# Performance work log

Measured on AMD Instinct MI355X. Metric: run time of the kernel, lower is better.

Reference implementation:

```python
import math
import jax, jax.numpy as jnp
import numpy as np

BATCH = 16384
N = 2048            # in_size = out_size, power of 2
LOG_N = 11          # log2(N)
NSTACKS = 1
NBLOCKS = 1


def setup_inputs() -> dict:
    key = jax.random.key(0)
    k1, k2, k3 = jax.random.split(key, 3)
    x = jax.random.normal(k1, (BATCH, N), jnp.float32)
    # init='randn': twiddle ~ N(0,1) / sqrt(2)
    twiddle = jax.random.normal(
        k2, (NSTACKS, NBLOCKS, LOG_N, N // 2, 2, 2), jnp.float32) / jnp.sqrt(jnp.float32(2.0))
    bound = 1.0 / math.sqrt(N)  # nn.Linear-style bias init, in_size = N
    bias = jax.random.uniform(k3, (N,), jnp.float32, -bound, bound)
    return {"x": x, "twiddle": twiddle, "bias": bias}


def butterfly_multiply(twiddle, x, increasing_stride=True):
    # twiddle: (S, n_blocks, log_n, n//2, 2, 2);  x: (B, S, n)
    B, S, n = x.shape
    n_blocks, log_n = twiddle.shape[1], twiddle.shape[2]
    out = x
    cur = increasing_stride
    for block in range(n_blocks):
        for idx in range(log_n):
            log_stride = idx if cur else log_n - 1 - idx
            s = 1 << log_stride
            g = n // (2 * s)  # number of butterfly groups at this stride
            # t: (S, g, s, 2, 2); pair axis j contracts against input halves
            t = twiddle[:, block, idx].reshape(S, g, s, 2, 2)
            xr = out.reshape(B, S, g, 2, s)
            out = jnp.einsum('kgsij,bkgjs->bkgis', t, xr).reshape(B, S, n)
        cur = not cur
    return out


def reference(x, twiddle, bias):
    B = x.shape[0]
    # pre_process: flatten batch dims, expand over nstacks
    out = jnp.broadcast_to(x[:, None, :], (B, NSTACKS, N))
    out = butterfly_multiply(twiddle, out, increasing_stride=True)
    # post_process: flatten stacks, truncate to out_size, add bias
    out = out.reshape(B, NSTACKS * N)[:, :N] + bias
    return out
```

## Files before the change

### kernel.cpp

```cpp
#include <hip/hip_runtime.h>


constexpr int BATCH = 16384;
constexpr int N = 2048;
constexpr int ROWS = 2;
constexpr int WPB = 4;
constexpr int BLOCK = 64 * WPB;
constexpr int GRID = BATCH / (ROWS * WPB);

#define SCHED_FENCE() asm volatile("" ::: "memory")

__device__ __forceinline__ int swz(int a) {
    return a ^ (((a >> 5) & 1) << 2) ^ (((a >> 6) & 1) << 3);
}

template <int M>
__device__ __forceinline__ float part_xor(float x) {
    if constexpr (M == 1)
        return __int_as_float(__builtin_amdgcn_mov_dpp(__float_as_int(x), 0xB1, 0xF, 0xF, true));
    else if constexpr (M == 2)
        return __int_as_float(__builtin_amdgcn_mov_dpp(__float_as_int(x), 0x4E, 0xF, 0xF, true));
    else if constexpr (M == 4)
        return __int_as_float(__builtin_amdgcn_ds_swizzle(__float_as_int(x), 0x101F));
    else if constexpr (M == 8)
        return __int_as_float(__builtin_amdgcn_ds_swizzle(__float_as_int(x), 0x201F));
    else if constexpr (M == 16)
        return __int_as_float(__builtin_amdgcn_ds_swizzle(__float_as_int(x), 0x401F));
    else
        return __shfl_xor(x, 32, 64);
}

template <int ST>
__device__ __forceinline__ void mid_stage(float (&v)[ROWS][32], const float* twb, int lane) {
    constexpr int s = 1 << ST;
    constexpr int m = 1 << (ST - 1);
    const int hiHalf = (lane >> (ST - 1)) & 1;
    const int l2 = lane * 2;
    #pragma unroll
    for (int k = 0; k < 32; ++k) {
        const int e = (k >> 1) * 128 + l2 + (k & 1);
        const int p = ((e >> (ST + 1)) << ST) | (e & (s - 1));
        const int a = swz(4 * p + 2 * hiHalf);
        const float2 t2 = *(const float2*)(twb + a);
        #pragma unroll
        for (int rr = 0; rr < ROWS; ++rr) {
            const float mine = v[rr][k];
            const float part = part_xor<m>(mine);
            const float lo = hiHalf ? part : mine;
            const float hi = hiHalf ? mine : part;
            v[rr][k] = fmaf(t2.x, lo, t2.y * hi);
        }
        if ((k & 3) == 3) SCHED_FENCE();
    }
}

template <int ST>
__device__ __forceinline__ void hi_stage(float (&v)[ROWS][32], const float* twb, int lane) {
    constexpr int s = 1 << ST;
    constexpr int rm = 1 << (ST - 7);
    const int l2 = lane * 2;
    #pragma unroll
    for (int r = 0; r < 16; ++r) {
        if (r & rm) continue;
        #pragma unroll
        for (int j = 0; j < 2; ++j) {
            const int e = r * 128 + l2 + j;
            const int p = ((e >> (ST + 1)) << ST) | (e & (s - 1));
            const int a = swz(4 * p);
            const float4 t4 = *(const float4*)(twb + a);
            const int klo = 2 * r + j;
            const int khi = 2 * (r + rm) + j;
            #pragma unroll
            for (int rr = 0; rr < ROWS; ++rr) {
                const float lo = v[rr][klo];
                const float hi = v[rr][khi];
                v[rr][klo] = fmaf(t4.x, lo, t4.y * hi);
                v[rr][khi] = fmaf(t4.z, lo, t4.w * hi);
            }
        }
        if ((r & 1) == 1) SCHED_FENCE();
    }
}

__global__ __launch_bounds__(BLOCK, 1)
void butterfly_kernel(const float* __restrict__ x,
                      const float* __restrict__ tw,
                      const float* __restrict__ bias,
                      float* __restrict__ out)
{
    __shared__ __align__(16) float lds[2][4096];
    const int tid = threadIdx.x;
    const int lane = tid & 63;
    const int w = tid >> 6;
    const int wid = blockIdx.x * WPB + w;
    const size_t row0 = (size_t)wid * ROWS;
    const int l2 = lane * 2;

    auto stage_tw = [&](int st, int buf) {
        const float* base = tw + (st << 12);
        #pragma unroll
        for (int i = 0; i < 4; ++i) {
            const int s = i * 256 + (w << 6) + lane;
            const int g = s ^ ((s >> 3) & 1) ^ (((s >> 4) & 1) << 1);
            __builtin_amdgcn_global_load_lds(
                (const __attribute__((address_space(1))) void*)(base + 4 * g),
                (__attribute__((address_space(3))) void*)(&lds[buf][(i * 256 + (w << 6)) * 4]),
                16, 0, 0);
        }
    };

    stage_tw(1, 1);

    float v[ROWS][32];

    #pragma unroll
    for (int rr = 0; rr < ROWS; ++rr) {
        const float* src = x + (row0 + rr) * N + l2;
        #pragma unroll
        for (int r = 0; r < 16; ++r) {
            const float2 f = *(const float2*)(src + r * 128);
            v[rr][2*r]   = f.x;
            v[rr][2*r+1] = f.y;
        }
    }

    #pragma unroll
    for (int r = 0; r < 16; ++r) {
        const float4 t4 = *(const float4*)(tw + 4 * (r * 64 + lane));
        #pragma unroll
        for (int rr = 0; rr < ROWS; ++rr) {
            const float lo = v[rr][2*r];
            const float hi = v[rr][2*r+1];
            v[rr][2*r]   = fmaf(t4.x, lo, t4.y * hi);
            v[rr][2*r+1] = fmaf(t4.z, lo, t4.w * hi);
        }
        if ((r & 3) == 3) SCHED_FENCE();
    }
    __syncthreads();

    stage_tw(2, 0);  mid_stage<1>(v, &lds[1][0], lane); __syncthreads();
    stage_tw(3, 1);  mid_stage<2>(v, &lds[0][0], lane); __syncthreads();
    stage_tw(4, 0);  mid_stage<3>(v, &lds[1][0], lane); __syncthreads();
    stage_tw(5, 1);  mid_stage<4>(v, &lds[0][0], lane); __syncthreads();
    stage_tw(6, 0);  mid_stage<5>(v, &lds[1][0], lane); __syncthreads();
    stage_tw(7, 1);  mid_stage<6>(v, &lds[0][0], lane); __syncthreads();
    stage_tw(8, 0);  hi_stage<7>(v, &lds[1][0], lane);  __syncthreads();
    stage_tw(9, 1);  hi_stage<8>(v, &lds[0][0], lane);  __syncthreads();
    stage_tw(10, 0); hi_stage<9>(v, &lds[1][0], lane);  __syncthreads();
    hi_stage<10>(v, &lds[0][0], lane);

    #pragma unroll
    for (int r = 0; r < 16; ++r) {
        const float2 b = *(const float2*)(bias + r * 128 + l2);
        #pragma unroll
        for (int rr = 0; rr < ROWS; ++rr) {
            float2 o;
            o.x = v[rr][2*r]   + b.x;
            o.y = v[rr][2*r+1] + b.y;
            *(float2*)(out + (row0 + rr) * N + r * 128 + l2) = o;
        }
    }
}

extern "C" void kernel_launch(void* const* d_in, const int* in_sizes, int n_in,
                              void* d_out, int out_size, void* d_ws, size_t ws_size,
                              hipStream_t stream) {
    const float* x    = (const float*)d_in[0];
    const float* tw   = (const float*)d_in[1];
    const float* bias = (const float*)d_in[2];
    float* out = (float*)d_out;

    butterfly_kernel<<<GRID, BLOCK, 0, stream>>>(x, tw, bias, out);
}
```

Baseline: 336.8 us.

## Read twiddles directly from global memory, drop LDS staging, process four rows per wave

Removes the double-buffered LDS staging of twiddle factors and the per-stage block barriers, so each wave loads twiddles directly from global memory (through cache). Rows per wave double to amortize each twiddle load over more batch rows, and the mid-stage butterfly precomputes per-lane coefficients to avoid selects. The trade-off is higher register pressure, fewer blocks, and exposing global/L2 latency on twiddle loads instead of LDS reads.

```diff
diff --git a/kernel.cpp b/kernel.cpp
--- a/kernel.cpp
+++ b/kernel.cpp
@@ -3,16 +3,12 @@
 
 constexpr int BATCH = 16384;
 constexpr int N = 2048;
-constexpr int ROWS = 2;
+constexpr int ROWS = 4;
 constexpr int WPB = 4;
 constexpr int BLOCK = 64 * WPB;
 constexpr int GRID = BATCH / (ROWS * WPB);
 
 #define SCHED_FENCE() asm volatile("" ::: "memory")
-
-__device__ __forceinline__ int swz(int a) {
-    return a ^ (((a >> 5) & 1) << 2) ^ (((a >> 6) & 1) << 3);
-}
 
 template <int M>
 __device__ __forceinline__ float part_xor(float x) {
@@ -31,7 +27,7 @@
 }
 
 template <int ST>
-__device__ __forceinline__ void mid_stage(float (&v)[ROWS][32], const float* twb, int lane) {
+__device__ __forceinline__ void mid_stage(float (&v)[ROWS][32], const float* twst, int lane) {
     constexpr int s = 1 << ST;
     constexpr int m = 1 << (ST - 1);
     const int hiHalf = (lane >> (ST - 1)) & 1;
@@ -40,22 +36,21 @@
     for (int k = 0; k < 32; ++k) {
         const int e = (k >> 1) * 128 + l2 + (k & 1);
         const int p = ((e >> (ST + 1)) << ST) | (e & (s - 1));
-        const int a = swz(4 * p + 2 * hiHalf);
-        const float2 t2 = *(const float2*)(twb + a);
+        const float2 t2 = *(const float2*)(twst + 4 * p + 2 * hiHalf);
+        const float cm = hiHalf ? t2.y : t2.x;
+        const float cp = hiHalf ? t2.x : t2.y;
         #pragma unroll
         for (int rr = 0; rr < ROWS; ++rr) {
             const float mine = v[rr][k];
             const float part = part_xor<m>(mine);
-            const float lo = hiHalf ? part : mine;
-            const float hi = hiHalf ? mine : part;
-            v[rr][k] = fmaf(t2.x, lo, t2.y * hi);
+            v[rr][k] = fmaf(cm, mine, cp * part);
         }
-        if ((k & 3) == 3) SCHED_FENCE();
+        if ((k & 7) == 7) SCHED_FENCE();
     }
 }
 
 template <int ST>
-__device__ __forceinline__ void hi_stage(float (&v)[ROWS][32], const float* twb, int lane) {
+__device__ __forceinline__ void hi_stage(float (&v)[ROWS][32], const float* twst, int lane) {
     constexpr int s = 1 << ST;
     constexpr int rm = 1 << (ST - 7);
     const int l2 = lane * 2;
@@ -66,8 +61,7 @@
         for (int j = 0; j < 2; ++j) {
             const int e = r * 128 + l2 + j;
             const int p = ((e >> (ST + 1)) << ST) | (e & (s - 1));
-            const int a = swz(4 * p);
-            const float4 t4 = *(const float4*)(twb + a);
+            const float4 t4 = *(const float4*)(twst + 4 * p);
             const int klo = 2 * r + j;
             const int khi = 2 * (r + rm) + j;
             #pragma unroll
@@ -88,28 +82,12 @@
                       const float* __restrict__ bias,
                       float* __restrict__ out)
 {
-    __shared__ __align__(16) float lds[2][4096];
     const int tid = threadIdx.x;
     const int lane = tid & 63;
     const int w = tid >> 6;
     const int wid = blockIdx.x * WPB + w;
     const size_t row0 = (size_t)wid * ROWS;
     const int l2 = lane * 2;
-
-    auto stage_tw = [&](int st, int buf) {
-        const float* base = tw + (st << 12);
-        #pragma unroll
-        for (int i = 0; i < 4; ++i) {
-            const int s = i * 256 + (w << 6) + lane;
-            const int g = s ^ ((s >> 3) & 1) ^ (((s >> 4) & 1) << 1);
-            __builtin_amdgcn_global_load_lds(
-                (const __attribute__((address_space(1))) void*)(base + 4 * g),
-                (__attribute__((address_space(3))) void*)(&lds[buf][(i * 256 + (w << 6)) * 4]),
-                16, 0, 0);
-        }
-    };
-
-    stage_tw(1, 1);
 
     float v[ROWS][32];
 
@@ -136,18 +114,18 @@
         }
         if ((r & 3) == 3) SCHED_FENCE();
     }
-    __syncthreads();
 
-    stage_tw(2, 0);  mid_stage<1>(v, &lds[1][0], lane); __syncthreads();
-    stage_tw(3, 1);  mid_stage<2>(v, &lds[0][0], lane); __syncthreads();
-    stage_tw(4, 0);  mid_stage<3>(v, &lds[1][0], lane); __syncthreads();
-    stage_tw(5, 1);  mid_stage<4>(v, &lds[0][0], lane); __syncthreads();
-    stage_tw(6, 0);  mid_stage<5>(v, &lds[1][0], lane); __syncthreads();
-    stage_tw(7, 1);  mid_stage<6>(v, &lds[0][0], lane); __syncthreads();
-    stage_tw(8, 0);  hi_stage<7>(v, &lds[1][0], lane);  __syncthreads();
-    stage_tw(9, 1);  hi_stage<8>(v, &lds[0][0], lane);  __syncthreads();
-    stage_tw(10, 0); hi_stage<9>(v, &lds[1][0], lane);  __syncthreads();
-    hi_stage<10>(v, &lds[0][0], lane);
+    mid_stage<1>(v, tw + (1 << 12), lane);
+    mid_stage<2>(v, tw + (2 << 12), lane);
+    mid_stage<3>(v, tw + (3 << 12), lane);
+    mid_stage<4>(v, tw + (4 << 12), lane);
+    mid_stage<5>(v, tw + (5 << 12), lane);
+    mid_stage<6>(v, tw + (6 << 12), lane);
+
+    hi_stage<7>(v, tw + (7 << 12), lane);
+    hi_stage<8>(v, tw + (8 << 12), lane);
+    hi_stage<9>(v, tw + (9 << 12), lane);
+    hi_stage<10>(v, tw + (10 << 12), lane);
 
     #pragma unroll
     for (int r = 0; r < 16; ++r) {
```

Measured after the change: 323.4 us. 4.0% less time.
